# Optimization experiments

Measured on AMD Instinct MI355X. Metric: run time of the kernel, lower is better.

Reference implementation:

```python
import jax, jax.numpy as jnp
import numpy as np

B, EMBED, HIDDEN, NH, D, H, W = 8, 384, 512, 32, 12, 32, 32  # attn_size D = EMBED // NH
SCALE = float(D) ** -0.5


def conv1x1(x, Wm, b):
    # 1x1 conv == per-pixel linear: x (B,Cin,H,W), Wm (Cout,Cin), b (Cout,)
    return jnp.einsum('bchw,oc->bohw', x, Wm) + b[None, :, None, None]


def mha(qc, kc, vc):
    # qc/kc/vc: (B, EMBED, H, W); tokens = H*W, heads = NH, head_dim = D
    HW = H * W
    def split(t):
        return t.reshape(B, NH, D, HW).transpose(0, 1, 3, 2)  # (B, nh, HW, d)
    q = split(qc) * SCALE
    k = split(kc)
    v = split(vc)
    w = jax.nn.softmax(jnp.einsum('bhnd,bhmd->bhnm', q, k), axis=-1)  # (B,nh,HW,HW)
    f = jnp.einsum('bhnm,bhmd->bhnd', w, v)  # (B,nh,HW,d)
    # (B,nh,HW,d) -> (B,HW,nh,d) -> (B,H,W,C) -> (B,C,H,W), matching torch view
    return f.transpose(0, 2, 1, 3).reshape(B, H, W, NH * D).transpose(0, 3, 1, 2)


def setup_inputs() -> dict:
    key = jax.random.key(0)
    ks = jax.random.split(key, 18)
    def p(k, shape):
        return jax.random.normal(k, shape, dtype=jnp.float32) * 0.02
    return {
        'x': jax.random.normal(ks[0], (B, EMBED, H, W), dtype=jnp.float32),
        'x_bpf': jax.random.normal(ks[1], (B, EMBED, H, W), dtype=jnp.float32),
        'Wq': p(ks[2], (EMBED, EMBED)), 'bq': p(ks[3], (EMBED,)),
        'Wk': p(ks[4], (EMBED, EMBED)), 'bk': p(ks[5], (EMBED,)),
        'Wv': p(ks[6], (EMBED, EMBED)), 'bv': p(ks[7], (EMBED,)),
        'Wq_bpf': p(ks[8], (EMBED, EMBED)), 'bq_bpf': p(ks[9], (EMBED,)),
        'Wk_bpf': p(ks[10], (EMBED, EMBED)), 'bk_bpf': p(ks[11], (EMBED,)),
        'Wv_bpf': p(ks[12], (EMBED, EMBED)), 'bv_bpf': p(ks[13], (EMBED,)),
        'Wo': p(ks[14], (HIDDEN, 2 * EMBED)), 'bo': p(ks[15], (HIDDEN,)),
    }


def reference(x, x_bpf, Wq, bq, Wk, bk, Wv, bv, Wq_bpf, bq_bpf, Wk_bpf, bk_bpf, Wv_bpf, bv_bpf, Wo, bo):
    q = conv1x1(x, Wq, bq)
    k = conv1x1(x, Wk, bk)
    v = conv1x1(x, Wv, bv)
    q_bpf = conv1x1(x_bpf, Wq_bpf, bq_bpf)
    k_bpf = conv1x1(x_bpf, Wk_bpf, bk_bpf)
    v_bpf = conv1x1(x_bpf, Wv_bpf, bv_bpf)
    # branch 1: query from bpf stream, key/value from x stream, residual to x
    f = mha(q_bpf, k, v) + x
    # branch 2: query from x stream, key/value from bpf stream, residual to x_bpf
    f_bpf = mha(q, k_bpf, v_bpf) + x_bpf
    fused = jnp.concatenate([f, f_bpf], axis=1)  # (B, 2*EMBED, H, W)
    return conv1x1(fused, Wo, bo)  # (B, HIDDEN, H, W)
```

## Files before the change

kernel.cpp:

```cpp
#include <hip/hip_runtime.h>
#include <hip/hip_bf16.h>

#define BB 8
#define EMBED 384
#define NH 32
#define HD 12
#define HWN 1024
#define HIDDEN 512
#define KTOT 1536
#define SCALE 0.28867513459481287f

typedef __attribute__((ext_vector_type(8))) unsigned short ushort8;
typedef __attribute__((ext_vector_type(8))) short short8;
typedef __attribute__((ext_vector_type(4))) float f32x4;
typedef __attribute__((ext_vector_type(16))) float f32x16;
typedef __attribute__((ext_vector_type(4))) unsigned short ushort4v;
typedef __attribute__((ext_vector_type(2))) unsigned int uint2v;

static __device__ __forceinline__ float bf2f(unsigned short u) {
    return __uint_as_float(((unsigned int)u) << 16);
}
static __device__ __forceinline__ unsigned short f2bf(float f) {
    unsigned int u = __float_as_uint(f);
    u = u + 0x7FFFu + ((u >> 16) & 1u);
    return (unsigned short)(u >> 16);
}
static __device__ __forceinline__ unsigned int cvt_pk_bf16(float lo, float hi) {
    unsigned int r;
    asm("v_cvt_pk_bf16_f32 %0, %1, %2" : "=v"(r) : "v"(lo), "v"(hi));
    return r;
}

struct WConv {
    const float* src[7];
    unsigned short* dst[7];
    int start[8];
};

__global__ __launch_bounds__(256) void k_bf16_all(WConv wc) {
    int i = blockIdx.x * 256 + threadIdx.x;
    if (i >= wc.start[7]) return;
    int p = 0;
#pragma unroll
    for (int j = 1; j < 7; ++j) p += (i >= wc.start[j]);
    const int e = i - wc.start[p];
    const f32x4 v = reinterpret_cast<const f32x4*>(wc.src[p])[e];
    ushort4v o;
#pragma unroll
    for (int j = 0; j < 4; ++j) o[j] = f2bf(v[j]);
    if (p == 6) {
        const int row = e / 192, cc = e % 192;
        ushort4v* d = reinterpret_cast<ushort4v*>(wc.dst[6]);
        d[row * 384 + cc] = o;
        d[row * 384 + 192 + cc] = o;
    } else {
        reinterpret_cast<ushort4v*>(wc.dst[p])[e] = o;
    }
}

__global__ __launch_bounds__(256) void k_transpose(const float* __restrict__ x0, const float* __restrict__ x1,
                                                   unsigned short* __restrict__ fused2) {
    __shared__ float tile[32][33];
    const int z = blockIdx.z;
    const int s = z >> 3, b = z & 7;
    const float* src = (s ? x1 : x0) + (size_t)b * EMBED * HWN;
    unsigned short* dst = fused2 + (size_t)b * HWN * KTOT + 768 + s * 384;
    const int c0 = blockIdx.x * 32;
    const int n0 = blockIdx.y * 32;
    const int tc = threadIdx.x & 31;
    const int tr = threadIdx.x >> 5;
#pragma unroll
    for (int p = 0; p < 4; ++p) {
        int r = tr + p * 8;
        tile[r][tc] = src[(size_t)(c0 + r) * HWN + n0 + tc];
    }
    __syncthreads();
#pragma unroll
    for (int p = 0; p < 4; ++p) {
        int r = tr + p * 8;
        dst[(size_t)(n0 + r) * KTOT + c0 + tc] = f2bf(tile[tc][r]);
    }
}

template <bool F32OUT>
static __device__ __forceinline__ void gemm_core(const unsigned short* __restrict__ A, int lda,
                                                 const unsigned short* __restrict__ Bt, int ldb,
                                                 const float* __restrict__ bias,
                                                 unsigned short* __restrict__ outBf,
                                                 float* __restrict__ outF,
                                                 int K, int bx, int by) {
    __shared__ unsigned short As[64][72];
    __shared__ unsigned short Bs[64][72];
    const int t = threadIdx.x;
    const int lane = t & 63;
    const int wid = t >> 6;
    const int wr = wid >> 1, wc = wid & 1;
    const int o0 = bx * 64, n0 = by * 64;
    const int lrow = t >> 2;
    const int lseg = t & 3;

    f32x4 acc[2][2] = {};

    for (int k0 = 0; k0 < K; k0 += 64) {
        const ushort8* ga = reinterpret_cast<const ushort8*>(A + (size_t)(o0 + lrow) * lda + k0 + lseg * 16);
        const ushort8* gb = reinterpret_cast<const ushort8*>(Bt + (size_t)(n0 + lrow) * ldb + k0 + lseg * 16);
        ushort8 a0 = ga[0], a1 = ga[1];
        ushort8 b0 = gb[0], b1 = gb[1];
        *reinterpret_cast<ushort8*>(&As[lrow][lseg * 16]) = a0;
        *reinterpret_cast<ushort8*>(&As[lrow][lseg * 16 + 8]) = a1;
        *reinterpret_cast<ushort8*>(&Bs[lrow][lseg * 16]) = b0;
        *reinterpret_cast<ushort8*>(&Bs[lrow][lseg * 16 + 8]) = b1;
        __syncthreads();
#pragma unroll
        for (int kk = 0; kk < 2; ++kk) {
            const int ko = kk * 32 + ((lane >> 4) << 3);
            short8 af[2], bfv[2];
            af[0]  = *reinterpret_cast<const short8*>(&As[wr * 32 + (lane & 15)][ko]);
            af[1]  = *reinterpret_cast<const short8*>(&As[wr * 32 + 16 + (lane & 15)][ko]);
            bfv[0] = *reinterpret_cast<const short8*>(&Bs[wc * 32 + (lane & 15)][ko]);
            bfv[1] = *reinterpret_cast<const short8*>(&Bs[wc * 32 + 16 + (lane & 15)][ko]);
#pragma unroll
            for (int i = 0; i < 2; ++i)
#pragma unroll
                for (int j = 0; j < 2; ++j)
                    acc[i][j] = __builtin_amdgcn_mfma_f32_16x16x32_bf16(af[i], bfv[j], acc[i][j], 0, 0, 0);
        }
        __syncthreads();
    }
#pragma unroll
    for (int i = 0; i < 2; ++i) {
#pragma unroll
        for (int j = 0; j < 2; ++j) {
            const int ob = o0 + wr * 32 + i * 16 + ((lane >> 4) << 2);
            const int n  = n0 + wc * 32 + j * 16 + (lane & 15);
#pragma unroll
            for (int r = 0; r < 4; ++r) {
                const int o = ob + r;
                float v = acc[i][j][r] + bias[o];
                if constexpr (F32OUT) outF[(size_t)o * HWN + n] = v;
                else                  outBf[(size_t)o * HWN + n] = f2bf(v);
            }
        }
    }
}

struct QkvTable {
    const unsigned short* W[6];
    const float* bias[6];
    const unsigned short* fused2;
    unsigned short* out[6];
};

__global__ __launch_bounds__(256) void k_gemm_qkv(QkvTable tab) {
    const int z = blockIdx.z;
    const int b = z / 6, p = z % 6;
    const unsigned short* Bt = tab.fused2 + (size_t)b * HWN * KTOT + 768 + (p / 3) * 384;
    gemm_core<false>(tab.W[p], EMBED, Bt, KTOT, tab.bias[p],
                     tab.out[p] + (size_t)b * EMBED * HWN, nullptr,
                     EMBED, blockIdx.x, blockIdx.y);
}

__global__ __launch_bounds__(256) void k_gemm_out(const unsigned short* __restrict__ Wo2,
                                                  const unsigned short* __restrict__ fused2,
                                                  const float* __restrict__ bo,
                                                  float* __restrict__ out) {
    const int b = blockIdx.z;
    gemm_core<true>(Wo2, KTOT, fused2 + (size_t)b * HWN * KTOT, KTOT, bo,
                    nullptr, out + (size_t)b * HIDDEN * HWN,
                    KTOT, blockIdx.x, blockIdx.y);
}

#define OT_STRIDE 416
__global__ __launch_bounds__(256) void k_attn_mfma(const unsigned short* __restrict__ qc,
                                                   const unsigned short* __restrict__ kc,
                                                   const unsigned short* __restrict__ vc,
                                                   const unsigned short* __restrict__ qcb,
                                                   const unsigned short* __restrict__ kcb,
                                                   const unsigned short* __restrict__ vcb,
                                                   unsigned short* __restrict__ fused2) {
    __shared__ unsigned short Ks[256][18];
    __shared__ unsigned short Vs[13][264];

    const int bid = blockIdx.x;
    const int inst = bid & 511, qt = bid >> 9;
    const int branch = inst >> 8, b = (inst >> 5) & 7, h = inst & 31;
    const unsigned short* Qg = branch ? qc : qcb;
    const unsigned short* Kg = branch ? kcb : kc;
    const unsigned short* Vg = branch ? vcb : vc;
    const int coff = branch ? 384 : 0;
    const size_t base = ((size_t)b * EMBED + h * HD) * HWN;
    const int t = threadIdx.x;
    const int lane = t & 63, w = t >> 6;
    const int q31 = lane & 31, hi = lane >> 5;
    const int n0 = qt * 256;
    const float C2 = SCALE * 1.4426950408889634f;

    short8 qf[2] = {};
#pragma unroll
    for (int i = 0; i < 2; ++i) {
        const int qg = n0 + i * 128 + w * 32 + q31;
#pragma unroll
        for (int j = 0; j < 8; ++j) {
            const int d = hi * 8 + j;
            if (d < HD)
                qf[i][j] = (short)f2bf(bf2f(Qg[base + (size_t)d * HWN + qg]) * C2);
        }
    }

    f32x16 acc[2], z16;
#pragma unroll
    for (int r = 0; r < 16; ++r) { acc[0][r] = 0.f; acc[1][r] = 0.f; z16[r] = 0.f; }
    const int vrow = (q31 < HD) ? q31 : 12;

    for (int phase = 0; phase < 4; ++phase) {
        const int m0 = phase << 8;
        __syncthreads();
        {
            const size_t kb = base + (size_t)(4 * w) * HWN + m0;
#pragma unroll
            for (int it = 0; it < 4; ++it) {
                const int m = it * 64 + lane;
                unsigned int da = 0, db = 0;
                if (w < 3) {
                    da = (unsigned int)Kg[kb + m] | ((unsigned int)Kg[kb + HWN + m] << 16);
                    db = (unsigned int)Kg[kb + 2 * HWN + m] | ((unsigned int)Kg[kb + 3 * HWN + m] << 16);
                }
                unsigned int* p = reinterpret_cast<unsigned int*>(&Ks[m][w * 4]);
                p[0] = da;
                p[1] = db;
            }
        }
        if (w < 3) {
#pragma unroll
            for (int r2 = 0; r2 < 2; ++r2) {
                const int d = 4 * w + 2 * r2 + (lane >> 5);
                const int col = (lane & 31) * 8;
                *reinterpret_cast<ushort8*>(&Vs[d][col]) =
                    *reinterpret_cast<const ushort8*>(&Vg[base + (size_t)d * HWN + m0 + col]);
            }
        } else if (lane < 32) {
            ushort8 ones;
#pragma unroll
            for (int j = 0; j < 8; ++j) ones[j] = 0x3F80;
            *reinterpret_cast<ushort8*>(&Vs[12][lane * 8]) = ones;
        }
        __syncthreads();

        for (int mc = 0; mc < 8; ++mc) {
            const int mb = mc << 5;
            union { short8 v; unsigned int u[4]; } kf;
            {
                const unsigned int* kp = reinterpret_cast<const unsigned int*>(&Ks[mb + q31][hi * 8]);
                kf.u[0] = kp[0]; kf.u[1] = kp[1]; kf.u[2] = kp[2]; kf.u[3] = kp[3];
            }
            union { short8 v; uint2v u2[2]; } vf1, vf2;
            vf1.u2[0] = *reinterpret_cast<const uint2v*>(&Vs[vrow][mb + hi * 4]);
            vf1.u2[1] = *reinterpret_cast<const uint2v*>(&Vs[vrow][mb + 8 + hi * 4]);
            vf2.u2[0] = *reinterpret_cast<const uint2v*>(&Vs[vrow][mb + 16 + hi * 4]);
            vf2.u2[1] = *reinterpret_cast<const uint2v*>(&Vs[vrow][mb + 24 + hi * 4]);
#pragma unroll
            for (int i = 0; i < 2; ++i) {
                const f32x16 s = __builtin_amdgcn_mfma_f32_32x32x16_bf16(kf.v, qf[i], z16, 0, 0, 0);
                union { short8 v; unsigned int u[4]; } p1, p2;
#pragma unroll
                for (int r = 0; r < 4; ++r) {
                    p1.u[r] = cvt_pk_bf16(__builtin_amdgcn_exp2f(s[2 * r]),
                                          __builtin_amdgcn_exp2f(s[2 * r + 1]));
                    p2.u[r] = cvt_pk_bf16(__builtin_amdgcn_exp2f(s[8 + 2 * r]),
                                          __builtin_amdgcn_exp2f(s[8 + 2 * r + 1]));
                }
                acc[i] = __builtin_amdgcn_mfma_f32_32x32x16_bf16(p1.v, vf1.v, acc[i], 0, 0, 0);
                acc[i] = __builtin_amdgcn_mfma_f32_32x32x16_bf16(p2.v, vf2.v, acc[i], 0, 0, 0);
            }
        }
    }

    float invq[2][16];
#pragma unroll
    for (int i = 0; i < 2; ++i)
#pragma unroll
        for (int r = 0; r < 16; ++r)
            invq[i][r] = 1.0f / __shfl(acc[i][r], (lane & 32) | 12);

    __syncthreads();
#pragma unroll
    for (int i = 0; i < 2; ++i) {
        unsigned short* OtW = &Ks[0][0] + (i * 4 + w) * OT_STRIDE;
        if (q31 < HD) {
#pragma unroll
            for (int r2 = 0; r2 < 8; ++r2) {
                const int r = 2 * r2;
                const int q = (r & 3) + 8 * (r >> 2) + 4 * hi;
                const unsigned int dw = (unsigned int)f2bf(acc[i][r] * invq[i][r]) |
                                        ((unsigned int)f2bf(acc[i][r + 1] * invq[i][r + 1]) << 16);
                *reinterpret_cast<unsigned int*>(&OtW[q31 * 32 + q]) = dw;
            }
        }
    }
    __syncthreads();
    {
        const int q = t;
        const int obi = ((q >> 7) * 4) + ((q >> 5) & 3);
        const int ql = q & 31;
        const unsigned short* Osrc = &Ks[0][0] + obi * OT_STRIDE + ql;
        unsigned int dwv[6];
#pragma unroll
        for (int dp = 0; dp < 6; ++dp)
            dwv[dp] = (unsigned int)Osrc[(2 * dp) * 32] | ((unsigned int)Osrc[(2 * dp + 1) * 32] << 16);
        unsigned int* dst = reinterpret_cast<unsigned int*>(
            fused2 + ((size_t)b * HWN + n0 + q) * KTOT + coff + h * HD);
#pragma unroll
        for (int dp = 0; dp < 6; ++dp) dst[dp] = dwv[dp];
    }
}

extern "C" void kernel_launch(void* const* d_in, const int* in_sizes, int n_in,
                              void* d_out, int out_size, void* d_ws, size_t ws_size,
                              hipStream_t stream) {
    (void)in_sizes; (void)n_in; (void)out_size; (void)ws_size;
    const float* x   = (const float*)d_in[0];
    const float* xbp = (const float*)d_in[1];
    const float* Wq  = (const float*)d_in[2];  const float* bq  = (const float*)d_in[3];
    const float* Wk  = (const float*)d_in[4];  const float* bk  = (const float*)d_in[5];
    const float* Wv  = (const float*)d_in[6];  const float* bv  = (const float*)d_in[7];
    const float* Wqb = (const float*)d_in[8];  const float* bqb = (const float*)d_in[9];
    const float* Wkb = (const float*)d_in[10]; const float* bkb = (const float*)d_in[11];
    const float* Wvb = (const float*)d_in[12]; const float* bvb = (const float*)d_in[13];
    const float* Wo  = (const float*)d_in[14]; const float* bo  = (const float*)d_in[15];
    float* out = (float*)d_out;

    char* ws = (char*)d_ws;
    size_t off = 0;
    auto alloc = [&](size_t bytes) -> void* {
        void* p = ws + off;
        off = (off + bytes + 255) & ~(size_t)255;
        return p;
    };
    unsigned short* wbf[6];
    for (int i = 0; i < 6; ++i) wbf[i] = (unsigned short*)alloc((size_t)EMBED * EMBED * 2);
    unsigned short* wo2 = (unsigned short*)alloc((size_t)HIDDEN * KTOT * 2);
    unsigned short* qkv[6];
    for (int i = 0; i < 6; ++i) qkv[i] = (unsigned short*)alloc((size_t)BB * EMBED * HWN * 2);
    unsigned short* fused2 = (unsigned short*)alloc((size_t)BB * HWN * KTOT * 2);

    WConv wc;
    const float* wsrc[7] = {Wq, Wk, Wv, Wqb, Wkb, Wvb, Wo};
    unsigned short* wdst[7] = {wbf[0], wbf[1], wbf[2], wbf[3], wbf[4], wbf[5], wo2};
    int acc4 = 0;
    for (int i = 0; i < 7; ++i) {
        const int n = (i < 6) ? EMBED * EMBED : HIDDEN * 768;
        wc.src[i] = wsrc[i];
        wc.dst[i] = wdst[i];
        wc.start[i] = acc4;
        acc4 += n / 4;
    }
    wc.start[7] = acc4;
    k_bf16_all<<<(acc4 + 255) / 256, 256, 0, stream>>>(wc);

    k_transpose<<<dim3(EMBED / 32, HWN / 32, 16), 256, 0, stream>>>(x, xbp, fused2);

    QkvTable tab;
    tab.W[0] = wbf[0]; tab.W[1] = wbf[1]; tab.W[2] = wbf[2];
    tab.W[3] = wbf[3]; tab.W[4] = wbf[4]; tab.W[5] = wbf[5];
    tab.bias[0] = bq; tab.bias[1] = bk; tab.bias[2] = bv;
    tab.bias[3] = bqb; tab.bias[4] = bkb; tab.bias[5] = bvb;
    tab.fused2 = fused2;
    for (int i = 0; i < 6; ++i) tab.out[i] = qkv[i];
    k_gemm_qkv<<<dim3(EMBED / 64, HWN / 64, BB * 6), 256, 0, stream>>>(tab);

    k_attn_mfma<<<dim3(2048), 256, 0, stream>>>(qkv[0], qkv[1], qkv[2], qkv[3], qkv[4], qkv[5],
                                                fused2);

    k_gemm_out<<<dim3(HIDDEN / 64, HWN / 64, BB), 256, 0, stream>>>(wo2, fused2, bo, out);
}
```

Measured before the change: 169.7 us.

## Enlarge GEMM tiles to 128x128 and stage operands via direct global-to-LDS loads

Both projection GEMMs now use 128x128 output tiles, with each wave computing a 64x64 sub-tile of 4x4 MFMA fragments instead of 2x2. Operand tiles are copied with global_load_lds (direct global-to-LDS DMA) when the builtin exists, otherwise with plain vector loads, and the LDS padding is removed. The aim is more operand reuse per LDS load and fewer register round-trips. In exchange the grids get smaller (QKV goes to 3x8x48 blocks, the output GEMM to 4x8x8=256 blocks), which may underfill the many CUs, and the unpadded LDS rows may cause bank conflicts on fragment reads.

```diff
diff --git a/kernel.cpp b/kernel.cpp
--- a/kernel.cpp
+++ b/kernel.cpp
@@ -30,6 +30,17 @@
     asm("v_cvt_pk_bf16_f32 %0, %1, %2" : "=v"(r) : "v"(lo), "v"(hi));
     return r;
 }
+
+#if __has_builtin(__builtin_amdgcn_global_load_lds)
+#define HAVE_GLOAD_LDS 1
+static __device__ __forceinline__ void gl_lds16(const unsigned short* g, unsigned short* l) {
+    __builtin_amdgcn_global_load_lds(
+        (const __attribute__((address_space(1))) unsigned int*)g,
+        (__attribute__((address_space(3))) unsigned int*)l, 16, 0, 0);
+}
+#else
+#define HAVE_GLOAD_LDS 0
+#endif
 
 struct WConv {
     const float* src[7];
@@ -83,56 +94,63 @@
 }
 
 template <bool F32OUT>
-static __device__ __forceinline__ void gemm_core(const unsigned short* __restrict__ A, int lda,
-                                                 const unsigned short* __restrict__ Bt, int ldb,
-                                                 const float* __restrict__ bias,
-                                                 unsigned short* __restrict__ outBf,
-                                                 float* __restrict__ outF,
-                                                 int K, int bx, int by) {
-    __shared__ unsigned short As[64][72];
-    __shared__ unsigned short Bs[64][72];
+static __device__ __forceinline__ void gemm128(const unsigned short* __restrict__ A, int lda,
+                                               const unsigned short* __restrict__ Bt, int ldb,
+                                               const float* __restrict__ bias,
+                                               unsigned short* __restrict__ outBf,
+                                               float* __restrict__ outF,
+                                               int K, int bx, int by) {
+    __shared__ unsigned short As[128][64];
+    __shared__ unsigned short Bs[128][64];
     const int t = threadIdx.x;
     const int lane = t & 63;
-    const int wid = t >> 6;
-    const int wr = wid >> 1, wc = wid & 1;
-    const int o0 = bx * 64, n0 = by * 64;
-    const int lrow = t >> 2;
-    const int lseg = t & 3;
-
-    f32x4 acc[2][2] = {};
+    const int w = t >> 6;
+    const int wr = w >> 1, wc = w & 1;
+    const int o0 = bx * 128, n0 = by * 128;
+    const int srow = lane >> 3;
+    const int scol = (lane & 7) * 8;
+
+    f32x4 acc[4][4] = {};
 
     for (int k0 = 0; k0 < K; k0 += 64) {
-        const ushort8* ga = reinterpret_cast<const ushort8*>(A + (size_t)(o0 + lrow) * lda + k0 + lseg * 16);
-        const ushort8* gb = reinterpret_cast<const ushort8*>(Bt + (size_t)(n0 + lrow) * ldb + k0 + lseg * 16);
-        ushort8 a0 = ga[0], a1 = ga[1];
-        ushort8 b0 = gb[0], b1 = gb[1];
-        *reinterpret_cast<ushort8*>(&As[lrow][lseg * 16]) = a0;
-        *reinterpret_cast<ushort8*>(&As[lrow][lseg * 16 + 8]) = a1;
-        *reinterpret_cast<ushort8*>(&Bs[lrow][lseg * 16]) = b0;
-        *reinterpret_cast<ushort8*>(&Bs[lrow][lseg * 16 + 8]) = b1;
+#pragma unroll
+        for (int i = 0; i < 4; ++i) {
+            const int c = w * 4 + i;
+            const int r = c * 8 + srow;
+#if HAVE_GLOAD_LDS
+            gl_lds16(A + (size_t)(o0 + r) * lda + k0 + scol, &As[c * 8][0]);
+            gl_lds16(Bt + (size_t)(n0 + r) * ldb + k0 + scol, &Bs[c * 8][0]);
+#else
+            *reinterpret_cast<ushort8*>(&As[r][scol]) =
+                *reinterpret_cast<const ushort8*>(A + (size_t)(o0 + r) * lda + k0 + scol);
+            *reinterpret_cast<ushort8*>(&Bs[r][scol]) =
+                *reinterpret_cast<const ushort8*>(Bt + (size_t)(n0 + r) * ldb + k0 + scol);
+#endif
+        }
         __syncthreads();
 #pragma unroll
         for (int kk = 0; kk < 2; ++kk) {
             const int ko = kk * 32 + ((lane >> 4) << 3);
-            short8 af[2], bfv[2];
-            af[0]  = *reinterpret_cast<const short8*>(&As[wr * 32 + (lane & 15)][ko]);
-            af[1]  = *reinterpret_cast<const short8*>(&As[wr * 32 + 16 + (lane & 15)][ko]);
-            bfv[0] = *reinterpret_cast<const short8*>(&Bs[wc * 32 + (lane & 15)][ko]);
-            bfv[1] = *reinterpret_cast<const short8*>(&Bs[wc * 32 + 16 + (lane & 15)][ko]);
-#pragma unroll
-            for (int i = 0; i < 2; ++i)
-#pragma unroll
-                for (int j = 0; j < 2; ++j)
-                    acc[i][j] = __builtin_amdgcn_mfma_f32_16x16x32_bf16(af[i], bfv[j], acc[i][j], 0, 0, 0);
+            short8 af[4], bf[4];
+#pragma unroll
+            for (int i = 0; i < 4; ++i) {
+                af[i] = *reinterpret_cast<const short8*>(&As[wr * 64 + i * 16 + (lane & 15)][ko]);
+                bf[i] = *reinterpret_cast<const short8*>(&Bs[wc * 64 + i * 16 + (lane & 15)][ko]);
+            }
+#pragma unroll
+            for (int i = 0; i < 4; ++i)
+#pragma unroll
+                for (int j = 0; j < 4; ++j)
+                    acc[i][j] = __builtin_amdgcn_mfma_f32_16x16x32_bf16(af[i], bf[j], acc[i][j], 0, 0, 0);
         }
         __syncthreads();
     }
 #pragma unroll
-    for (int i = 0; i < 2; ++i) {
-#pragma unroll
-        for (int j = 0; j < 2; ++j) {
-            const int ob = o0 + wr * 32 + i * 16 + ((lane >> 4) << 2);
-            const int n  = n0 + wc * 32 + j * 16 + (lane & 15);
+    for (int i = 0; i < 4; ++i) {
+#pragma unroll
+        for (int j = 0; j < 4; ++j) {
+            const int ob = o0 + wr * 64 + i * 16 + ((lane >> 4) << 2);
+            const int n  = n0 + wc * 64 + j * 16 + (lane & 15);
 #pragma unroll
             for (int r = 0; r < 4; ++r) {
                 const int o = ob + r;
@@ -155,9 +173,9 @@
     const int z = blockIdx.z;
     const int b = z / 6, p = z % 6;
     const unsigned short* Bt = tab.fused2 + (size_t)b * HWN * KTOT + 768 + (p / 3) * 384;
-    gemm_core<false>(tab.W[p], EMBED, Bt, KTOT, tab.bias[p],
-                     tab.out[p] + (size_t)b * EMBED * HWN, nullptr,
-                     EMBED, blockIdx.x, blockIdx.y);
+    gemm128<false>(tab.W[p], EMBED, Bt, KTOT, tab.bias[p],
+                   tab.out[p] + (size_t)b * EMBED * HWN, nullptr,
+                   EMBED, blockIdx.x, blockIdx.y);
 }
 
 __global__ __launch_bounds__(256) void k_gemm_out(const unsigned short* __restrict__ Wo2,
@@ -165,9 +183,9 @@
                                                   const float* __restrict__ bo,
                                                   float* __restrict__ out) {
     const int b = blockIdx.z;
-    gemm_core<true>(Wo2, KTOT, fused2 + (size_t)b * HWN * KTOT, KTOT, bo,
-                    nullptr, out + (size_t)b * HIDDEN * HWN,
-                    KTOT, blockIdx.x, blockIdx.y);
+    gemm128<true>(Wo2, KTOT, fused2 + (size_t)b * HWN * KTOT, KTOT, bo,
+                  nullptr, out + (size_t)b * HIDDEN * HWN,
+                  KTOT, blockIdx.x, blockIdx.y);
 }
 
 #define OT_STRIDE 416
@@ -366,10 +384,10 @@
     tab.bias[3] = bqb; tab.bias[4] = bkb; tab.bias[5] = bvb;
     tab.fused2 = fused2;
     for (int i = 0; i < 6; ++i) tab.out[i] = qkv[i];
-    k_gemm_qkv<<<dim3(EMBED / 64, HWN / 64, BB * 6), 256, 0, stream>>>(tab);
+    k_gemm_qkv<<<dim3(EMBED / 128, HWN / 128, BB * 6), 256, 0, stream>>>(tab);
 
     k_attn_mfma<<<dim3(2048), 256, 0, stream>>>(qkv[0], qkv[1], qkv[2], qkv[3], qkv[4], qkv[5],
                                                 fused2);
 
-    k_gemm_out<<<dim3(HIDDEN / 64, HWN / 64, BB), 256, 0, stream>>>(wo2, fused2, bo, out);
-}
+    k_gemm_out<<<dim3(HIDDEN / 128, HWN / 128, BB), 256, 0, stream>>>(wo2, fused2, bo, out);
+}
```

New measurement: 166.9 us (median of 2 runs). No clear change (-1.6%).
